# Optimization experiments

Hardware: AMD Instinct MI355X
Metric: run time of the kernel (lower is better)

The kernel has to match this reference:

```python
import jax, jax.numpy as jnp
import numpy as np

N_PRED = 10000
N_GT = 1000
NUM_CLASSES = 80
IMG_H = 800
IMG_W = 1333
EPS = 1e-12
ALPHA, GAMMA, CLS_W = 0.25, 2.0, 2.0
L1_W, IOU_W = 5.0, 2.0
CENTER_RADIUS = 2.5
CAND_TOPK = 5


def _make_boxes(key, n, w, h):
    k1, k2 = jax.random.split(key)
    cxcy = jax.random.uniform(k1, (n, 2)) * jnp.array([w, h], jnp.float32)
    wh = jax.random.uniform(k2, (n, 2)) * 190.0 + 10.0
    return jnp.concatenate([cxcy - wh / 2, cxcy + wh / 2], axis=1).astype(jnp.float32)


def setup_inputs() -> dict:
    key = jax.random.key(0)
    k1, k2, k3, k4 = jax.random.split(key, 4)
    return {
        'pred_logits': jax.random.normal(k1, (N_PRED, NUM_CLASSES), jnp.float32),
        'pred_boxes': _make_boxes(k2, N_PRED, IMG_W, IMG_H),
        'gt_bboxes': _make_boxes(k3, N_GT, IMG_W, IMG_H),
        'gt_labels': jax.random.randint(k4, (N_GT,), 0, NUM_CLASSES),
        'img_h': IMG_H,
        'img_w': IMG_W,
    }


def _pairwise_iou_giou(pred, gt):
    area_p = (pred[:, 2] - pred[:, 0]) * (pred[:, 3] - pred[:, 1])
    area_g = (gt[:, 2] - gt[:, 0]) * (gt[:, 3] - gt[:, 1])
    lt = jnp.maximum(pred[:, None, :2], gt[None, :, :2])
    rb = jnp.minimum(pred[:, None, 2:], gt[None, :, 2:])
    wh = jnp.clip(rb - lt, 0.0)
    inter = wh[..., 0] * wh[..., 1]                       # [N,G]
    union = area_p[:, None] + area_g[None, :] - inter
    iou = inter / jnp.maximum(union, EPS)
    elt = jnp.minimum(pred[:, None, :2], gt[None, :, :2])
    erb = jnp.maximum(pred[:, None, 2:], gt[None, :, 2:])
    ewh = jnp.clip(erb - elt, 0.0)
    enclose = ewh[..., 0] * ewh[..., 1]
    giou = iou - (enclose - union) / jnp.maximum(enclose, EPS)
    return iou, giou


def _center_info(pred, gt):
    # pred/gt in xyxy; uses pred box centers, strict inequalities as in source
    pcx = (pred[:, 0] + pred[:, 2]) * 0.5
    pcy = (pred[:, 1] + pred[:, 3]) * 0.5
    gx1, gy1, gx2, gy2 = gt[:, 0], gt[:, 1], gt[:, 2], gt[:, 3]
    in_boxes = ((pcx[:, None] > gx1) & (pcx[:, None] < gx2) &
                (pcy[:, None] > gy1) & (pcy[:, None] < gy2))
    gcx, gcy = (gx1 + gx2) * 0.5, (gy1 + gy2) * 0.5
    gw, gh = gx2 - gx1, gy2 - gy1
    r = CENTER_RADIUS
    in_centers = ((pcx[:, None] > gcx - r * gw) & (pcx[:, None] < gcx + r * gw) &
                  (pcy[:, None] > gcy - r * gh) & (pcy[:, None] < gcy + r * gh))
    valid = in_boxes.any(1) | in_centers.any(1)
    return valid, in_boxes & in_centers


def _compute_cost_and_ious(pred_logits, pred_boxes, gt_bboxes, gt_labels, img_h, img_w):
    # FocalLossCost
    p = jax.nn.sigmoid(pred_logits)
    neg = -jnp.log1p(-(p - EPS)) * (1 - ALPHA) * p ** GAMMA
    pos = -jnp.log(p + EPS) * ALPHA * (1 - p) ** GAMMA
    cls_cost = (pos - neg)[:, gt_labels] * CLS_W            # [N,G]
    # BBoxL1Cost (normalized by image size)
    factor = jnp.array([img_w, img_h, img_w, img_h], jnp.float32)
    l1_cost = jnp.sum(jnp.abs(pred_boxes[:, None, :] / factor -
                              gt_bboxes[None, :, :] / factor), -1) * L1_W
    # IoUCost (giou) + pairwise ious for dynamic-k
    ious, giou = _pairwise_iou_giou(pred_boxes, gt_bboxes)
    iou_cost = -giou * IOU_W
    valid_mask, in_boxes_and_center = _center_info(pred_boxes, gt_bboxes)
    cost = cls_cost + l1_cost + iou_cost + jnp.where(in_boxes_and_center, 0.0, 100.0)
    cost = cost + jnp.where(valid_mask, 0.0, 10000.0)[:, None]
    return cost, ious


def _dynamic_k_matching(cost, ious):
    n, g = cost.shape
    k = min(CAND_TOPK, n)
    topk_ious, _ = jax.lax.top_k(ious.T, k)                 # [G,k]
    dynamic_ks = jnp.maximum(topk_ious.sum(1).astype(jnp.int32), 1)
    _, idx = jax.lax.top_k(-cost.T, k)                      # [G,k] smallest costs per gt
    vals = (jnp.arange(k)[None, :] < dynamic_ks[:, None]).astype(cost.dtype)
    cols = jnp.broadcast_to(jnp.arange(g)[:, None], (g, k))
    mm = jnp.zeros_like(cost).at[idx, cols].max(vals)       # scatter 1s per gt column
    # resolve priors matched to >1 gt (note: mask is reused stale inside the loop, as in source)
    prior_mask = mm.sum(1) > 1
    cmin = jnp.argmin(cost, axis=1)
    mm = jnp.where(prior_mask[:, None], jax.nn.one_hot(cmin, g, dtype=cost.dtype), mm)

    def cond(state):
        m, _ = state
        return jnp.any(m.sum(0) == 0)

    def body(state):
        m, c = state
        matched_q = m.sum(1) > 0
        c = c + 100000.0 * matched_q[:, None].astype(c.dtype)
        unmatched = m.sum(0) == 0
        pos = jnp.argmin(c, axis=0)                         # [G]
        oh = jax.nn.one_hot(pos, n, dtype=c.dtype).T        # [N,G]
        m = jnp.where(unmatched[None, :], oh, m)
        cmin2 = jnp.argmin(c, axis=1)
        m_fix = jnp.where(prior_mask[:, None], jax.nn.one_hot(cmin2, g, dtype=c.dtype), m)
        m = jnp.where(jnp.any(m.sum(1) > 1), m_fix, m)
        return (m, c)

    mm, _ = jax.lax.while_loop(cond, body, (mm, cost))
    fg_mask = mm.sum(1) > 0
    matched = jnp.argmax(mm, axis=1).astype(jnp.int32)
    return fg_mask, jnp.where(fg_mask, matched, 0)


def reference(pred_logits, pred_boxes, gt_bboxes, gt_labels, img_h, img_w):
    cost, ious = _compute_cost_and_ious(pred_logits, pred_boxes, gt_bboxes,
                                        gt_labels, img_h, img_w)
    fg_mask, matched_gt = _dynamic_k_matching(cost, ious)
    # dense form: matched_gt[i] valid only where fg_mask[i] (fixed-shape version of
    # the original's compressed matched_gt_inds = mm[fg_mask].argmax(1))
    return fg_mask, matched_gt
```

## Files before the change

kernel.cpp:

```cpp
#include <hip/hip_runtime.h>
#include <cfloat>
#include <cmath>

#define NP 10000
#define NG 1000
#define NC 80
#define LMAX 6

#define S_MULTI 12
#define S_BODY  16
#define RI_BIG  0x3fffffff
#define KMAX    0xFFFFFFFFFFFFFFFFull

#define TKEY    0xC248000000000000ull

#define CMAIN   39
#define CTAIL   16

#define WCAP    384

__device__ __forceinline__ bool lexless(float av, int ai, float bv, int bi) {
    return (av < bv) || (av == bv && ai < bi);
}

__device__ __forceinline__ unsigned long long packkey(float v, int idx) {
    unsigned u = __float_as_uint(v);
    u ^= (unsigned)(((int)u) >> 31) | 0x80000000u;
    return ((unsigned long long)u << 32) | (unsigned)idx;
}
__device__ __forceinline__ int keyidx(unsigned long long k) {
    return (int)(unsigned)(k & 0xFFFFFFFFu);
}

__device__ __forceinline__ float inflate(float c, int k) {
    for (int q = 0; q < k; q++) c += 100000.0f;
    return c;
}

__device__ __forceinline__ void cost_iou(float4 p, float4 pn, float4 pi,
        float4 g, float4 cb, float4 Gn, float ga, float clsv,
        float& cc_out, float& iou_out) {
#pragma clang fp contract(off)
    float wx = fminf(p.z, g.z) - fmaxf(p.x, g.x); wx = fmaxf(wx, 0.0f);
    float wy = fminf(p.w, g.w) - fmaxf(p.y, g.y); wy = fmaxf(wy, 0.0f);
    float inter = wx * wy;
    float uni = pi.z + ga - inter;
    float iou = inter / fmaxf(uni, 1e-12f);
    float ex = fmaxf(p.z, g.z) - fminf(p.x, g.x); ex = fmaxf(ex, 0.0f);
    float ey = fmaxf(p.w, g.w) - fminf(p.y, g.y); ey = fmaxf(ey, 0.0f);
    float enc = ex * ey;
    float giou = iou - (enc - uni) / fmaxf(enc, 1e-12f);
    float l1 = ((fabsf(pn.x - Gn.x) + fabsf(pn.y - Gn.y))
                + fabsf(pn.z - Gn.z)) + fabsf(pn.w - Gn.w);
    float cc = clsv + l1 * 5.0f;
    cc = cc + (-giou * 2.0f);
    bool inb = (pi.x > g.x && pi.x < g.z && pi.y > g.y && pi.y < g.w);
    bool inc = (pi.x > cb.x && pi.x < cb.z && pi.y > cb.y && pi.y < cb.w);
    cc = cc + ((inb && inc) ? 0.0f : 100.0f);
    cc = cc + pi.w;
    cc_out = cc; iou_out = iou;
}

__device__ __forceinline__ void ins5k(unsigned long long* kv,
        unsigned long long key) {
    if (key < kv[4]) {
        kv[4] = key;
#pragma unroll
        for (int t = 4; t > 0; t--)
            if (kv[t] < kv[t-1]) { unsigned long long tv = kv[t]; kv[t] = kv[t-1]; kv[t-1] = tv; }
    }
}
__device__ __forceinline__ void ins5i(float* iv, float iou) {
    if (iou > iv[4]) {
        iv[4] = iou;
#pragma unroll
        for (int t = 4; t > 0; t--)
            if (iv[t] > iv[t-1]) { float tv = iv[t]; iv[t] = iv[t-1]; iv[t-1] = tv; }
    }
}

#define CLS_TI 64
#define PB_CLS0 40
#define PB_G0   197
#define PB_V0   201
__global__ __launch_bounds__(256) void k_prep(const float* __restrict__ logits,
        const float* __restrict__ pb, const float* __restrict__ gb,
        const int* __restrict__ imgw, const int* __restrict__ imgh,
        float* __restrict__ clsval, float4* __restrict__ pnorm,
        float4* __restrict__ pinfo, float4* __restrict__ gcb,
        float4* __restrict__ gnm, float* __restrict__ gar,
        int* rowcnt, int* rowfirst, int* rowiter, int* prior, int* priorcol,
        int* colsum, int* scal)
{
    __shared__ float sl[CLS_TI * (NC + 1)];
    int b = blockIdx.x;
    if (b < PB_CLS0) {
        int i = b * 256 + threadIdx.x;
        if (i < NP) {
            rowcnt[i] = 0; rowfirst[i] = 0x7fffffff; rowiter[i] = RI_BIG;
            prior[i] = 0; priorcol[i] = 0;
        }
        if (i < NG) colsum[i] = 0;
        if (i < 32) scal[i] = 0;
    } else if (b < PB_G0) {
        int i0 = (b - PB_CLS0) * CLS_TI;
        bool full = (i0 + CLS_TI) <= NP;
        if (full) {
            const float* src = logits + (size_t)i0 * NC;
            for (int e = threadIdx.x; e < CLS_TI * NC; e += 256) {
                int di = e / NC, c = e - di * NC;
                sl[di * (NC + 1) + c] = src[e];
            }
        } else {
            for (int e = threadIdx.x; e < CLS_TI * NC; e += 256) {
                int di = e / NC, c = e - di * NC;
                int i = i0 + di;
                sl[di * (NC + 1) + c] = (i < NP) ? logits[(size_t)i * NC + c] : 0.0f;
            }
        }
        __syncthreads();
        for (int e = threadIdx.x; e < CLS_TI * NC; e += 256) {
            int c = e >> 6, di = e & 63;
            int i = i0 + di;
            if (i >= NP) continue;
            float x = sl[di * (NC + 1) + c];
            float p = 1.0f / (1.0f + expf(-x));
            float neg = -log1pf(-(p - 1e-12f)) * 0.75f * (p * p);
            float om = 1.0f - p;
            float pos = -logf(p + 1e-12f) * 0.25f * (om * om);
            clsval[(size_t)c * NP + i] = (pos - neg) * 2.0f;
        }
    } else if (b < PB_V0) {
#pragma clang fp contract(off)
        int j = (b - PB_G0) * 256 + threadIdx.x;
        if (j < NG) {
            float fw = (float)imgw[0], fh = (float)imgh[0];
            float4 g = ((const float4*)gb)[j];
            float gcx = (g.x + g.z) * 0.5f, gcy = (g.y + g.w) * 0.5f;
            float gw = g.z - g.x, gh = g.w - g.y;
            float4 cb; cb.x = gcx - 2.5f * gw; cb.y = gcy - 2.5f * gh;
            cb.z = gcx + 2.5f * gw; cb.w = gcy + 2.5f * gh;
            gcb[j] = cb;
            float4 Gn; Gn.x = g.x / fw; Gn.y = g.y / fh; Gn.z = g.z / fw; Gn.w = g.w / fh;
            gnm[j] = Gn;
            gar[j] = (g.z - g.x) * (g.w - g.y);
        }
    } else {
#pragma clang fp contract(off)
        int wave = threadIdx.x >> 6;
        int lane = threadIdx.x & 63;
        int i = (b - PB_V0) * 4 + wave;
        if (i >= NP) return;
        float4 p = ((const float4*)pb)[i];
        float pcx = (p.x + p.z) * 0.5f, pcy = (p.y + p.w) * 0.5f;
        int vb = 0, vc = 0;
        const float4* gb4 = (const float4*)gb;
        for (int jb = 0; jb < NG; jb += 64) {
            int j = jb + lane;
            if (j < NG) {
                float4 g = gb4[j];
                vb |= (pcx > g.x && pcx < g.z && pcy > g.y && pcy < g.w) ? 1 : 0;
                float gcx = (g.x + g.z) * 0.5f, gcy = (g.y + g.w) * 0.5f;
                float gw = g.z - g.x, gh = g.w - g.y;
                vc |= (pcx > gcx - 2.5f * gw && pcx < gcx + 2.5f * gw &&
                       pcy > gcy - 2.5f * gh && pcy < gcy + 2.5f * gh) ? 1 : 0;
            }
            if (__any(vb | vc)) break;
        }
        int any = __any(vb | vc) ? 1 : 0;
        if (lane == 0) {
            float fw = (float)imgw[0], fh = (float)imgh[0];
            float4 pn; pn.x = p.x / fw; pn.y = p.y / fh; pn.z = p.z / fw; pn.w = p.w / fh;
            pnorm[i] = pn;
            float4 pi4; pi4.x = pcx; pi4.y = pcy;
            pi4.z = (p.z - p.x) * (p.w - p.y);
            pi4.w = any ? 0.0f : 10000.0f;
            pinfo[i] = pi4;
        }
    }
}

__device__ __forceinline__ void tree57(unsigned long long* s_k, float* s_iv,
        int tid) {
    for (int w = 128; w > 0; w >>= 1) {
        if (tid < w) {
            int a = tid * 7, bb = (tid + w) * 7;
            unsigned long long ok[5]; float og[5];
            int pa = a, pbp = bb;
#pragma unroll
            for (int t = 0; t < 5; t++) {
                unsigned long long A = s_k[pa], B = s_k[pbp];
                if (A <= B) { ok[t] = A; pa++; } else { ok[t] = B; pbp++; }
            }
            int qa = a, qb = bb;
#pragma unroll
            for (int t = 0; t < 5; t++) {
                float A = s_iv[qa], B = s_iv[qb];
                if (A >= B) { og[t] = A; qa++; } else { og[t] = B; qb++; }
            }
#pragma unroll
            for (int t = 0; t < 5; t++) { s_k[a+t] = ok[t]; s_iv[a+t] = og[t]; }
        }
        __syncthreads();
    }
}

__global__ __launch_bounds__(256) void k_cost2(
        const float* __restrict__ pb, const float* __restrict__ gb,
        const int* __restrict__ glab, const float* __restrict__ clsval,
        const float4* __restrict__ pnorm, const float4* __restrict__ pinfo,
        const float4* __restrict__ gcb, const float4* __restrict__ gnm,
        const float* __restrict__ gar,
        int* __restrict__ rowcnt, int* __restrict__ rowfirst,
        int* __restrict__ rowiter, int* __restrict__ top5,
        int* __restrict__ dkarr)
{
    __shared__ unsigned long long s_k[256 * 7];
    __shared__ float s_iv[256 * 7];
    __shared__ int s_wcnt[4];
    int* s_list = (int*)s_iv;

    int j = blockIdx.x;
    int tid = threadIdx.x;
    int wid = tid >> 6;
    int ln  = tid & 63;
    float4 g  = ((const float4*)gb)[j];
    float4 cb = gcb[j];
    float4 Gn = gnm[j];
    float  ga = gar[j];
    const float* clscol = clsval + (size_t)glab[j] * NP;
    const float4* pb4 = (const float4*)pb;

    int wbase = 0;
    for (int k = 0; k <= CMAIN; k++) {
        if (k == CMAIN && tid >= CTAIL) break;
        int i = tid + k * 256;
        float4 p = pb4[i];
        bool o = (p.z > g.x) & (g.z > p.x) & (p.w > g.y) & (g.w > p.y);
        unsigned long long m = __ballot(o ? 1 : 0);
        if (o) {
            int slot = wbase + __popcll(m & ((1ull << ln) - 1ull));
            if (slot < WCAP) s_list[wid * WCAP + slot] = i;
        }
        wbase += __popcll(m);
    }
    if (ln == 0) s_wcnt[wid] = wbase;
    __syncthreads();
    int c0 = s_wcnt[0], c1 = s_wcnt[1], c2 = s_wcnt[2], c3 = s_wcnt[3];
    bool overflow = (c0 > WCAP) | (c1 > WCAP) | (c2 > WCAP) | (c3 > WCAP);

    unsigned long long kv[5]; float iv[5];
#pragma unroll
    for (int t = 0; t < 5; t++) { kv[t] = KMAX; iv[t] = overflow ? -1.0f : 0.0f; }

    if (!overflow) {
        for (int q = tid; q < c0; q += 256) {
            int i = s_list[q];
            float cc, iou;
            cost_iou(pb4[i], pnorm[i], pinfo[i], g, cb, Gn, ga, clscol[i], cc, iou);
            ins5k(kv, packkey(cc, i)); ins5i(iv, iou);
        }
        for (int q = tid; q < c1; q += 256) {
            int i = s_list[WCAP + q];
            float cc, iou;
            cost_iou(pb4[i], pnorm[i], pinfo[i], g, cb, Gn, ga, clscol[i], cc, iou);
            ins5k(kv, packkey(cc, i)); ins5i(iv, iou);
        }
        for (int q = tid; q < c2; q += 256) {
            int i = s_list[2 * WCAP + q];
            float cc, iou;
            cost_iou(pb4[i], pnorm[i], pinfo[i], g, cb, Gn, ga, clscol[i], cc, iou);
            ins5k(kv, packkey(cc, i)); ins5i(iv, iou);
        }
        for (int q = tid; q < c3; q += 256) {
            int i = s_list[3 * WCAP + q];
            float cc, iou;
            cost_iou(pb4[i], pnorm[i], pinfo[i], g, cb, Gn, ga, clscol[i], cc, iou);
            ins5k(kv, packkey(cc, i)); ins5i(iv, iou);
        }
    } else {
        for (int k = 0; k <= CMAIN; k++) {
            if (k == CMAIN && tid >= CTAIL) break;
            int i = tid + k * 256;
            float cc, iou;
            cost_iou(pb4[i], pnorm[i], pinfo[i], g, cb, Gn, ga, clscol[i], cc, iou);
            ins5k(kv, packkey(cc, i)); ins5i(iv, iou);
        }
    }
    __syncthreads();

    int base = tid * 7;
#pragma unroll
    for (int t = 0; t < 5; t++) { s_k[base+t] = kv[t]; s_iv[base+t] = iv[t]; }
    s_k[base+5] = KMAX; s_iv[base+5] = -2.0f;
    __syncthreads();
    tree57(s_k, s_iv, tid);

    bool redo = !overflow && (s_k[4] >= TKEY);
    __syncthreads();

    if (redo) {
#pragma unroll
        for (int t = 0; t < 5; t++) { kv[t] = KMAX; iv[t] = -1.0f; }
        for (int k = 0; k <= CMAIN; k++) {
            if (k == CMAIN && tid >= CTAIL) break;
            int i = tid + k * 256;
            float cc, iou;
            cost_iou(pb4[i], pnorm[i], pinfo[i], g, cb, Gn, ga, clscol[i], cc, iou);
            ins5k(kv, packkey(cc, i)); ins5i(iv, iou);
        }
#pragma unroll
        for (int t = 0; t < 5; t++) { s_k[base+t] = kv[t]; s_iv[base+t] = iv[t]; }
        s_k[base+5] = KMAX; s_iv[base+5] = -2.0f;
        __syncthreads();
        tree57(s_k, s_iv, tid);
    }

    if (tid == 0) {
        float s = (((s_iv[0] + s_iv[1]) + s_iv[2]) + s_iv[3]) + s_iv[4];
        int dk = (int)s;
        if (dk < 1) dk = 1;
        dkarr[j] = dk;
#pragma unroll
        for (int t = 0; t < 5; t++) top5[j * 5 + t] = keyidx(s_k[t]);
#pragma unroll
        for (int t = 0; t < 5; t++) {
            if (t < dk) {
                int r = keyidx(s_k[t]);
                atomicAdd(&rowcnt[r], 1);
                atomicMin(&rowfirst[r], j);
                atomicMin(&rowiter[r], -1);
            }
        }
    }
}

__global__ __launch_bounds__(256) void k_pfixsurv(const float* __restrict__ pb,
        const float* __restrict__ gb, const int* __restrict__ glab,
        const float* __restrict__ clsval,
        const float4* __restrict__ pnorm, const float4* __restrict__ pinfo,
        const float4* __restrict__ gcb, const float4* __restrict__ gnm,
        const float* __restrict__ gar,
        int* __restrict__ prior, int* __restrict__ priorcol,
        int* __restrict__ colsum,
        const int* __restrict__ rowcnt, const int* __restrict__ top5,
        const int* __restrict__ dkarr)
{
    int b = blockIdx.x;
    int tid = threadIdx.x;
    if (b >= 2500) {
        int j = (b - 2500) * 256 + tid;
        if (j >= NG) return;
        int c = 0;
        int dk = dkarr[j];
        for (int t = 0; t < dk; t++) if (rowcnt[top5[j * 5 + t]] == 1) c++;
        if (c) atomicAdd(&colsum[j], c);
        return;
    }
    __shared__ float rv[256]; __shared__ int ri[256];
    for (int q = 0; q < 4; q++) {
        int row = b * 4 + q;
        if (rowcnt[row] <= 1) continue;
        if (tid == 0) prior[row] = 1;
        float4 p = ((const float4*)pb)[row];
        float4 pn = pnorm[row];
        float4 pi4 = pinfo[row];
        float best = FLT_MAX; int bj = 0x7fffffff;
        for (int j = tid; j < NG; j += 256) {
            float cc, iou;
            cost_iou(p, pn, pi4, ((const float4*)gb)[j], gcb[j], gnm[j], gar[j],
                     clsval[(size_t)glab[j] * NP + row], cc, iou);
            if (lexless(cc, j, best, bj)) { best = cc; bj = j; }
        }
        rv[tid] = best; ri[tid] = bj; __syncthreads();
        for (int w = 128; w > 0; w >>= 1) {
            if (tid < w) {
                float ov = rv[tid + w]; int oi = ri[tid + w];
                if (lexless(ov, oi, rv[tid], ri[tid])) { rv[tid] = ov; ri[tid] = oi; }
            }
            __syncthreads();
        }
        if (tid == 0) {
            priorcol[row] = ri[0];
            atomicAdd(&colsum[ri[0]], 1);
        }
        __syncthreads();
    }
}

__global__ __launch_bounds__(256) void k_iterB(const float* __restrict__ pb,
        const float* __restrict__ gb, const int* __restrict__ glab,
        const float* __restrict__ clsval,
        const float4* __restrict__ pnorm, const float4* __restrict__ pinfo,
        const float4* __restrict__ gcb, const float4* __restrict__ gnm,
        const float* __restrict__ gar, const int* __restrict__ top5,
        int* __restrict__ rowiter, int* __restrict__ rowcnt,
        int* __restrict__ rowfirst, int* __restrict__ colsum,
        int* __restrict__ scal, int t)
{
    int j = blockIdx.x;
    if (colsum[j] != 0) return;
    int tid = threadIdx.x;
    if (tid == 0) scal[S_BODY + t] = 1;

    __shared__ int s_pos;
    if (tid == 0) {
        int pos = -1;
        for (int r = 0; r < 5; r++) {
            int i = top5[j * 5 + r];
            if (rowiter[i] >= t) { pos = i; break; }
        }
        s_pos = pos;
    }
    __syncthreads();
    int pos = s_pos;

    if (pos < 0) {
        float4 g  = ((const float4*)gb)[j];
        float4 cb = gcb[j];
        float4 Gn = gnm[j];
        float  ga = gar[j];
        const float* clscol = clsval + (size_t)glab[j] * NP;
        const float4* pb4 = (const float4*)pb;
        __shared__ float rv[256]; __shared__ int ri[256];
        float best = FLT_MAX; int bi = 0x7fffffff;
        for (int i = tid; i < NP; i += 256) {
            if (rowiter[i] < t) continue;
            float cc, iou;
            cost_iou(pb4[i], pnorm[i], pinfo[i], g, cb, Gn, ga, clscol[i], cc, iou);
            if (lexless(cc, i, best, bi)) { best = cc; bi = i; }
        }
        rv[tid] = best; ri[tid] = bi; __syncthreads();
        for (int w = 128; w > 0; w >>= 1) {
            if (tid < w) {
                float ov = rv[tid + w]; int oi = ri[tid + w];
                if (lexless(ov, oi, rv[tid], ri[tid])) { rv[tid] = ov; ri[tid] = oi; }
            }
            __syncthreads();
        }
        pos = ri[0];
    }

    if (tid == 0) {
        colsum[j] = 1;
        int old = atomicAdd(&rowcnt[pos], 1);
        if (old >= 1) scal[S_MULTI] = 1;
        atomicMin(&rowfirst[pos], j);
        atomicMin(&rowiter[pos], t);
    }
}

__global__ __launch_bounds__(256) void k_iterC(const float* __restrict__ pb,
        const float* __restrict__ gb, const int* __restrict__ glab,
        const float* __restrict__ clsval,
        const float4* __restrict__ pnorm, const float4* __restrict__ pinfo,
        const float4* __restrict__ gcb, const float4* __restrict__ gnm,
        const float* __restrict__ gar,
        const int* __restrict__ prior, const int* __restrict__ rowiter,
        int* __restrict__ priorcol, int* __restrict__ colsum,
        int* __restrict__ scal, int t)
{
    if (scal[S_BODY + t] == 0 || scal[S_MULTI] == 0) return;
    int b = blockIdx.x;
    int tid = threadIdx.x;
    __shared__ float rv[256]; __shared__ int ri[256];
    for (int q = 0; q < 4; q++) {
        int row = b * 4 + q;
        if (!prior[row]) continue;
        int k = t - rowiter[row]; if (k < 0) k = 0;
        float4 p = ((const float4*)pb)[row];
        float4 pn = pnorm[row];
        float4 pi4 = pinfo[row];
        float best = FLT_MAX; int bj = 0x7fffffff;
        for (int j = tid; j < NG; j += 256) {
            float cc, iou;
            cost_iou(p, pn, pi4, ((const float4*)gb)[j], gcb[j], gnm[j], gar[j],
                     clsval[(size_t)glab[j] * NP + row], cc, iou);
            float val = inflate(cc, k);
            if (lexless(val, j, best, bj)) { best = val; bj = j; }
        }
        rv[tid] = best; ri[tid] = bj; __syncthreads();
        for (int w = 128; w > 0; w >>= 1) {
            if (tid < w) {
                float ov = rv[tid + w]; int oi = ri[tid + w];
                if (lexless(ov, oi, rv[tid], ri[tid])) { rv[tid] = ov; ri[tid] = oi; }
            }
            __syncthreads();
        }
        if (tid == 0) {
            int nb = ri[0];
            int oldc = priorcol[row];
            if (nb != oldc) {
                atomicSub(&colsum[oldc], 1);
                atomicAdd(&colsum[nb], 1);
                priorcol[row] = nb;
            }
        }
        __syncthreads();
    }
}

__global__ __launch_bounds__(256) void k_final(const int* __restrict__ rowcnt,
        const int* __restrict__ prior, const int* __restrict__ priorcol,
        const int* __restrict__ rowfirst, int* __restrict__ out)
{
    int i = blockIdx.x * 256 + threadIdx.x;
    if (i >= NP) return;
    int fg = rowcnt[i] > 0;
    out[i] = fg ? 1 : 0;
    out[NP + i] = fg ? (prior[i] ? priorcol[i] : rowfirst[i]) : 0;
}

extern "C" void kernel_launch(void* const* d_in, const int* in_sizes, int n_in,
                              void* d_out, int out_size, void* d_ws, size_t ws_size,
                              hipStream_t stream)
{
    (void)in_sizes; (void)n_in; (void)out_size; (void)ws_size;
    const float* logits = (const float*)d_in[0];
    const float* pboxes = (const float*)d_in[1];
    const float* gboxes = (const float*)d_in[2];
    const int*   glab   = (const int*)d_in[3];
    const int*   imgh   = (const int*)d_in[4];
    const int*   imgw   = (const int*)d_in[5];
    int* out = (int*)d_out;

    char* w = (char*)d_ws;
    float*  clsval  = (float*)(w);
    float4* pnorm   = (float4*)(w + 3200000);
    float4* pinfo   = (float4*)(w + 3360000);
    float4* gcb     = (float4*)(w + 3520000);
    float4* gnm     = (float4*)(w + 3536000);
    float*  gar     = (float*)(w + 3552000);
    int* rowcnt     = (int*)(w + 3556000);
    int* rowfirst   = (int*)(w + 3596000);
    int* rowiter    = (int*)(w + 3636000);
    int* prior      = (int*)(w + 3676000);
    int* priorcol   = (int*)(w + 3716000);
    int* top5       = (int*)(w + 3756000);
    int* dkarr      = (int*)(w + 3776000);
    int* colsum     = (int*)(w + 3780000);
    int* scal       = (int*)(w + 3784000);

    hipLaunchKernelGGL(k_prep, dim3(2701), dim3(256), 0, stream,
                       logits, pboxes, gboxes, imgw, imgh,
                       clsval, pnorm, pinfo, gcb, gnm, gar,
                       rowcnt, rowfirst, rowiter, prior, priorcol, colsum, scal);
    hipLaunchKernelGGL(k_cost2, dim3(NG), dim3(256), 0, stream,
                       pboxes, gboxes, glab, clsval, pnorm, pinfo, gcb, gnm, gar,
                       rowcnt, rowfirst, rowiter, top5, dkarr);
    hipLaunchKernelGGL(k_pfixsurv, dim3(2504), dim3(256), 0, stream,
                       pboxes, gboxes, glab, clsval, pnorm, pinfo, gcb, gnm, gar,
                       prior, priorcol, colsum, rowcnt, top5, dkarr);
    for (int t = 0; t < LMAX; t++) {
        hipLaunchKernelGGL(k_iterB, dim3(NG), dim3(256), 0, stream,
                           pboxes, gboxes, glab, clsval, pnorm, pinfo, gcb, gnm, gar,
                           top5, rowiter, rowcnt, rowfirst, colsum, scal, t);
        hipLaunchKernelGGL(k_iterC, dim3(2500), dim3(256), 0, stream,
                           pboxes, gboxes, glab, clsval, pnorm, pinfo, gcb, gnm, gar,
                           prior, rowiter, priorcol, colsum, scal, t);
    }
    hipLaunchKernelGGL(k_final, dim3(40), dim3(256), 0, stream,
                       rowcnt, prior, priorcol, rowfirst, out);
}
```

Baseline: 159.6 us.

## Split per-GT cost top-5 across four prediction chunks and merge

The cost/top-k kernel now launches four blocks per ground-truth box, each scanning a quarter of the predictions and writing a partial top-5 key list and IoU list to workspace. A new small merge kernel combines the four partial lists per GT, computes dynamic k, and performs the row atomics. This raises parallelism from 1000 blocks to 4000 so the GPU is better occupied. In exchange it adds a kernel launch and a serial per-thread merge, and the redo/overflow thresholds now apply per chunk.

Result: slower. 163.1 us (+2.2%).

```diff
diff --git a/kernel.cpp b/kernel.cpp
--- a/kernel.cpp
+++ b/kernel.cpp
@@ -6,6 +6,10 @@
 #define NG 1000
 #define NC 80
 #define LMAX 6
+#define NCH 4
+#define CHSZ (NP / NCH)
+#define CMAIN 9
+#define CTAIL 196
 
 #define S_MULTI 12
 #define S_BODY  16
@@ -14,10 +18,7 @@
 
 #define TKEY    0xC248000000000000ull
 
-#define CMAIN   39
-#define CTAIL   16
-
-#define WCAP    384
+#define WCAP    448
 
 __device__ __forceinline__ bool lexless(float av, int ai, float bv, int bi) {
     return (av < bv) || (av == bv && ai < bi);
@@ -211,16 +212,15 @@
         const float4* __restrict__ pnorm, const float4* __restrict__ pinfo,
         const float4* __restrict__ gcb, const float4* __restrict__ gnm,
         const float* __restrict__ gar,
-        int* __restrict__ rowcnt, int* __restrict__ rowfirst,
-        int* __restrict__ rowiter, int* __restrict__ top5,
-        int* __restrict__ dkarr)
+        unsigned long long* __restrict__ pck, float* __restrict__ piv)
 {
     __shared__ unsigned long long s_k[256 * 7];
     __shared__ float s_iv[256 * 7];
     __shared__ int s_wcnt[4];
     int* s_list = (int*)s_iv;
 
-    int j = blockIdx.x;
+    int j = blockIdx.x >> 2;
+    int c = blockIdx.x & 3;
     int tid = threadIdx.x;
     int wid = tid >> 6;
     int ln  = tid & 63;
@@ -230,11 +230,12 @@
     float  ga = gar[j];
     const float* clscol = clsval + (size_t)glab[j] * NP;
     const float4* pb4 = (const float4*)pb;
+    int base_i = c * CHSZ;
 
     int wbase = 0;
     for (int k = 0; k <= CMAIN; k++) {
         if (k == CMAIN && tid >= CTAIL) break;
-        int i = tid + k * 256;
+        int i = base_i + tid + k * 256;
         float4 p = pb4[i];
         bool o = (p.z > g.x) & (g.z > p.x) & (p.w > g.y) & (g.w > p.y);
         unsigned long long m = __ballot(o ? 1 : 0);
@@ -281,7 +282,7 @@
     } else {
         for (int k = 0; k <= CMAIN; k++) {
             if (k == CMAIN && tid >= CTAIL) break;
-            int i = tid + k * 256;
+            int i = base_i + tid + k * 256;
             float cc, iou;
             cost_iou(pb4[i], pnorm[i], pinfo[i], g, cb, Gn, ga, clscol[i], cc, iou);
             ins5k(kv, packkey(cc, i)); ins5i(iv, iou);
@@ -304,7 +305,7 @@
         for (int t = 0; t < 5; t++) { kv[t] = KMAX; iv[t] = -1.0f; }
         for (int k = 0; k <= CMAIN; k++) {
             if (k == CMAIN && tid >= CTAIL) break;
-            int i = tid + k * 256;
+            int i = base_i + tid + k * 256;
             float cc, iou;
             cost_iou(pb4[i], pnorm[i], pinfo[i], g, cb, Gn, ga, clscol[i], cc, iou);
             ins5k(kv, packkey(cc, i)); ins5i(iv, iou);
@@ -317,21 +318,62 @@
     }
 
     if (tid == 0) {
-        float s = (((s_iv[0] + s_iv[1]) + s_iv[2]) + s_iv[3]) + s_iv[4];
-        int dk = (int)s;
-        if (dk < 1) dk = 1;
-        dkarr[j] = dk;
-#pragma unroll
-        for (int t = 0; t < 5; t++) top5[j * 5 + t] = keyidx(s_k[t]);
-#pragma unroll
-        for (int t = 0; t < 5; t++) {
-            if (t < dk) {
-                int r = keyidx(s_k[t]);
-                atomicAdd(&rowcnt[r], 1);
-                atomicMin(&rowfirst[r], j);
-                atomicMin(&rowiter[r], -1);
-            }
-        }
+        int ob = blockIdx.x * 5;
+#pragma unroll
+        for (int t = 0; t < 5; t++) { pck[ob + t] = s_k[t]; piv[ob + t] = s_iv[t]; }
+    }
+}
+
+__global__ __launch_bounds__(256) void k_costmerge(
+        const unsigned long long* __restrict__ pck, const float* __restrict__ piv,
+        int* __restrict__ rowcnt, int* __restrict__ rowfirst,
+        int* __restrict__ rowiter, int* __restrict__ top5,
+        int* __restrict__ dkarr)
+{
+    int j = blockIdx.x * 256 + threadIdx.x;
+    if (j >= NG) return;
+    int base = j * NCH * 5;
+    int h0 = 0, h1 = 0, h2 = 0, h3 = 0;
+    int besti[5];
+#pragma unroll
+    for (int r = 0; r < 5; r++) {
+        unsigned long long v0 = (h0 < 5) ? pck[base + h0]      : KMAX;
+        unsigned long long v1 = (h1 < 5) ? pck[base + 5 + h1]  : KMAX;
+        unsigned long long v2 = (h2 < 5) ? pck[base + 10 + h2] : KMAX;
+        unsigned long long v3 = (h3 < 5) ? pck[base + 15 + h3] : KMAX;
+        unsigned long long best = v0; int sel = 0;
+        if (v1 < best) { best = v1; sel = 1; }
+        if (v2 < best) { best = v2; sel = 2; }
+        if (v3 < best) { best = v3; sel = 3; }
+        besti[r] = keyidx(best);
+        h0 += (sel == 0); h1 += (sel == 1); h2 += (sel == 2); h3 += (sel == 3);
+    }
+    int g0 = 0, g1 = 0, g2 = 0, g3 = 0;
+    float ivm[5];
+#pragma unroll
+    for (int r = 0; r < 5; r++) {
+        float w0 = (g0 < 5) ? piv[base + g0]      : -2.0f;
+        float w1 = (g1 < 5) ? piv[base + 5 + g1]  : -2.0f;
+        float w2 = (g2 < 5) ? piv[base + 10 + g2] : -2.0f;
+        float w3 = (g3 < 5) ? piv[base + 15 + g3] : -2.0f;
+        float best = w0; int sel = 0;
+        if (w1 > best) { best = w1; sel = 1; }
+        if (w2 > best) { best = w2; sel = 2; }
+        if (w3 > best) { best = w3; sel = 3; }
+        ivm[r] = best;
+        g0 += (sel == 0); g1 += (sel == 1); g2 += (sel == 2); g3 += (sel == 3);
+    }
+    float s = (((ivm[0] + ivm[1]) + ivm[2]) + ivm[3]) + ivm[4];
+    int dk = (int)s;
+    if (dk < 1) dk = 1;
+    dkarr[j] = dk;
+#pragma unroll
+    for (int r = 0; r < 5; r++) top5[j * 5 + r] = besti[r];
+    for (int t = 0; t < dk; t++) {
+        int r = besti[t];
+        atomicAdd(&rowcnt[r], 1);
+        atomicMin(&rowfirst[r], j);
+        atomicMin(&rowiter[r], -1);
     }
 }
 
@@ -540,14 +582,18 @@
     int* dkarr      = (int*)(w + 3776000);
     int* colsum     = (int*)(w + 3780000);
     int* scal       = (int*)(w + 3784000);
+    unsigned long long* pck = (unsigned long long*)(w + 3784128);
+    float* piv      = (float*)(w + 3944128);
 
     hipLaunchKernelGGL(k_prep, dim3(2701), dim3(256), 0, stream,
                        logits, pboxes, gboxes, imgw, imgh,
                        clsval, pnorm, pinfo, gcb, gnm, gar,
                        rowcnt, rowfirst, rowiter, prior, priorcol, colsum, scal);
-    hipLaunchKernelGGL(k_cost2, dim3(NG), dim3(256), 0, stream,
+    hipLaunchKernelGGL(k_cost2, dim3(NG * NCH), dim3(256), 0, stream,
                        pboxes, gboxes, glab, clsval, pnorm, pinfo, gcb, gnm, gar,
-                       rowcnt, rowfirst, rowiter, top5, dkarr);
+                       pck, piv);
+    hipLaunchKernelGGL(k_costmerge, dim3(4), dim3(256), 0, stream,
+                       pck, piv, rowcnt, rowfirst, rowiter, top5, dkarr);
     hipLaunchKernelGGL(k_pfixsurv, dim3(2504), dim3(256), 0, stream,
                        pboxes, gboxes, glab, clsval, pnorm, pinfo, gcb, gnm, gar,
                        prior, priorcol, colsum, rowcnt, top5, dkarr);
```
